# Optimization experiments

Measured on AMD Instinct MI355X. Metric: run time of the kernel, lower is better.

Reference implementation:

```python
import jax, jax.numpy as jnp
import numpy as np

D = 1024
H = 16
EPS = 1e-5


def setup_inputs() -> dict:
    key = jax.random.key(0)
    ks = jax.random.split(key, 6)
    B, T, d = 4, 2048, D
    s = 0.02
    return {
        "x": jax.random.normal(ks[0], (B, T, d), jnp.float32),
        "w_attn": jax.random.normal(ks[1], (d, 3 * d), jnp.float32) * s,
        "w_o": jax.random.normal(ks[2], (d, d), jnp.float32) * s,
        "ln1_g": jnp.ones((d,), jnp.float32),
        "ln1_b": jnp.zeros((d,), jnp.float32),
        "ln2_g": jnp.ones((d,), jnp.float32),
        "ln2_b": jnp.zeros((d,), jnp.float32),
        "w_fc": jax.random.normal(ks[3], (d, 4 * d), jnp.float32) * s,
        "b_fc": jnp.zeros((4 * d,), jnp.float32),
        "w_proj": jax.random.normal(ks[4], (4 * d, d), jnp.float32) * s,
        "b_proj": jnp.zeros((d,), jnp.float32),
    }


def _layernorm(x, g, b):
    mu = jnp.mean(x, axis=-1, keepdims=True)
    var = jnp.mean(jnp.square(x - mu), axis=-1, keepdims=True)
    return (x - mu) * jax.lax.rsqrt(var + EPS) * g + b


def _attention(x, w_attn, w_o):
    B, T, d = x.shape
    hd = d // H
    qkv = x @ w_attn  # [B,T,3d]
    q, k, v = jnp.split(qkv, 3, axis=-1)
    q = q.reshape(B, T, H, hd).transpose(0, 2, 1, 3)  # [B,H,T,hd]
    k = k.reshape(B, T, H, hd).transpose(0, 2, 1, 3)
    v = v.reshape(B, T, H, hd).transpose(0, 2, 1, 3)
    att = jnp.einsum("bhqd,bhkd->bhqk", q, k) * (1.0 / np.sqrt(hd))
    mask = jnp.tril(jnp.ones((T, T), bool))
    att = jnp.where(mask, att, jnp.float32(-jnp.inf))
    att = jax.nn.softmax(att, axis=-1)
    y = jnp.einsum("bhqk,bhkd->bhqd", att, v)
    y = y.transpose(0, 2, 1, 3).reshape(B, T, d)
    return y @ w_o


def reference(x, w_attn, w_o, ln1_g, ln1_b, ln2_g, ln2_b, w_fc, b_fc, w_proj, b_proj):
    x = x + _attention(_layernorm(x, ln1_g, ln1_b), w_attn, w_o)
    h = _layernorm(x, ln2_g, ln2_b)
    h = jax.nn.gelu(h @ w_fc + b_fc, approximate=True)
    return x + h @ w_proj + b_proj
```

## Files before the change

kernel.cpp:

```cpp
#include <hip/hip_runtime.h>
#include <math.h>

#define D_MODEL 1024
#define NHEAD   16
#define HDIM    64
#define SEQ     2048
#define BATCH   4
#define NROWS   (BATCH*SEQ)

using bf16x8 = __attribute__((ext_vector_type(8))) short;
using bf16x4 = __attribute__((ext_vector_type(4))) short;
using f32x4  = __attribute__((ext_vector_type(4))) float;

__device__ __forceinline__ unsigned short f2bf(float f) {
    unsigned u = __float_as_uint(f);
    u += 0x7fffu + ((u >> 16) & 1u);
    return (unsigned short)(u >> 16);
}
__device__ __forceinline__ float bf2f(unsigned short h) {
    unsigned u = ((unsigned)h) << 16;
    return __uint_as_float(u);
}

#define ASYNC_COPY16(g, l) \
    __builtin_amdgcn_global_load_lds((__attribute__((address_space(1))) const void*)(g), \
                                     (__attribute__((address_space(3))) void*)(l), 16, 0, 0)

__global__ __launch_bounds__(256) void ln_kernel(const float* __restrict__ x,
                                                 const float* __restrict__ g,
                                                 const float* __restrict__ b,
                                                 unsigned short* __restrict__ out) {
    const int row = blockIdx.x;
    const int tid = threadIdx.x;
    const float4* x4 = (const float4*)(x + (size_t)row * D_MODEL);
    float4 v = x4[tid];
    float s  = v.x + v.y + v.z + v.w;
    float sq = v.x*v.x + v.y*v.y + v.z*v.z + v.w*v.w;
    #pragma unroll
    for (int off = 32; off >= 1; off >>= 1) {
        s  += __shfl_down(s,  off, 64);
        sq += __shfl_down(sq, off, 64);
    }
    __shared__ float rs[4], rq[4];
    const int wave = tid >> 6;
    if ((tid & 63) == 0) { rs[wave] = s; rq[wave] = sq; }
    __syncthreads();
    const float tot  = rs[0] + rs[1] + rs[2] + rs[3];
    const float totq = rq[0] + rq[1] + rq[2] + rq[3];
    const float mu   = tot * (1.0f / D_MODEL);
    const float var  = totq * (1.0f / D_MODEL) - mu * mu;
    const float rstd = rsqrtf(var + 1e-5f);
    const float4 gv = ((const float4*)g)[tid];
    const float4 bv = ((const float4*)b)[tid];
    unsigned short* o = out + (size_t)row * D_MODEL + tid * 4;
    o[0] = f2bf((v.x - mu) * rstd * gv.x + bv.x);
    o[1] = f2bf((v.y - mu) * rstd * gv.y + bv.y);
    o[2] = f2bf((v.z - mu) * rstd * gv.z + bv.z);
    o[3] = f2bf((v.w - mu) * rstd * gv.w + bv.w);
}

__global__ __launch_bounds__(256) void wt_kernel(const float* __restrict__ w,
                                                 unsigned short* __restrict__ wt,
                                                 int K, int N) {
    __shared__ float tile[32][33];
    const int n0 = blockIdx.x * 32, k0 = blockIdx.y * 32;
    const int tx = threadIdx.x & 31, ty = threadIdx.x >> 5;
    #pragma unroll
    for (int j = 0; j < 4; ++j)
        tile[ty + j * 8][tx] = w[(size_t)(k0 + ty + j * 8) * N + n0 + tx];
    __syncthreads();
    #pragma unroll
    for (int j = 0; j < 4; ++j)
        wt[(size_t)(n0 + ty + j * 8) * K + k0 + tx] = f2bf(tile[tx][ty + j * 8]);
}

template<bool GELU, bool OUT_BF16, bool QSCALE, bool PARTIAL>
__global__ __launch_bounds__(256) void gemm_bt(const unsigned short* __restrict__ A,
                                               const unsigned short* __restrict__ Bt,
                                               const float* __restrict__ bias,
                                               const float* __restrict__ resid,
                                               void* __restrict__ outp,
                                               int M, int N, int K, int Kslice) {
    __shared__ __align__(16) unsigned short As[128 * 32];
    __shared__ __align__(16) unsigned short Bs[128 * 32];

    const int tid  = threadIdx.x;
    const int lane = tid & 63;
    const int wave = __builtin_amdgcn_readfirstlane(tid >> 6);
    const int quad = lane >> 4, l16 = lane & 15;
    const int wm = wave >> 1, wn = wave & 1;
    const int m0 = blockIdx.y * 128, n0 = blockIdx.x * 128;
    const int kbeg = PARTIAL ? blockIdx.z * Kslice : 0;

    f32x4 acc[4][4] = {};

    const int rA = tid >> 2;
    const int p  = tid & 3;
    const int cs = (p ^ ((rA >> 1) & 3)) * 8;

    const unsigned short* Ag0 = A  + (size_t)(m0 + rA) * K + cs + kbeg;
    const unsigned short* Ag1 = A  + (size_t)(m0 + rA + 64) * K + cs + kbeg;
    const unsigned short* Bg0 = Bt + (size_t)(n0 + rA) * K + cs + kbeg;
    const unsigned short* Bg1 = Bt + (size_t)(n0 + rA + 64) * K + cs + kbeg;
    unsigned short* Al0 = As + tid * 8;
    unsigned short* Al1 = As + tid * 8 + 2048;
    unsigned short* Bl0 = Bs + tid * 8;
    unsigned short* Bl1 = Bs + tid * 8 + 2048;

    const int sw = (quad ^ ((l16 >> 1) & 3)) * 8;

    for (int kb = 0; kb < Kslice; kb += 32) {
        ASYNC_COPY16(Ag0 + kb, Al0);
        ASYNC_COPY16(Ag1 + kb, Al1);
        ASYNC_COPY16(Bg0 + kb, Bl0);
        ASYNC_COPY16(Bg1 + kb, Bl1);
        __syncthreads();

        bf16x8 a[4], b[4];
        #pragma unroll
        for (int i = 0; i < 4; ++i)
            a[i] = *(const bf16x8*)&As[(wm * 64 + i * 16 + l16) * 32 + sw];
        #pragma unroll
        for (int j = 0; j < 4; ++j)
            b[j] = *(const bf16x8*)&Bs[(wn * 64 + j * 16 + l16) * 32 + sw];
        #pragma unroll
        for (int i = 0; i < 4; ++i)
            #pragma unroll
            for (int j = 0; j < 4; ++j)
                acc[i][j] = __builtin_amdgcn_mfma_f32_16x16x32_bf16(a[i], b[j], acc[i][j], 0, 0, 0);
        __syncthreads();
    }

    unsigned short* outb = (unsigned short*)outp;
    if (PARTIAL) outb += (size_t)blockIdx.z * M * N;

    #pragma unroll
    for (int i = 0; i < 4; ++i)
      #pragma unroll
      for (int j = 0; j < 4; ++j)
        #pragma unroll
        for (int r = 0; r < 4; ++r) {
            const int row = m0 + wm * 64 + i * 16 + quad * 4 + r;
            const int col = n0 + wn * 64 + j * 16 + l16;
            float v = acc[i][j][r];
            if (PARTIAL) {
                outb[(size_t)row * N + col] = f2bf(v);
            } else {
                if (QSCALE && col < 1024) v *= 0.125f;
                if (bias) v += bias[col];
                if (GELU) {
                    const float u = 0.7978845608028654f * (v + 0.044715f * v * v * v);
                    const float e = __expf(2.0f * u);
                    v = 0.5f * v * (2.0f - 2.0f / (e + 1.0f));
                }
                if (resid) v += resid[(size_t)row * N + col];
                if (OUT_BF16) outb[(size_t)row * N + col] = f2bf(v);
                else          ((float*)outp)[(size_t)row * N + col] = v;
            }
        }
}

__global__ __launch_bounds__(256, 2) void gemm_big(const unsigned short* __restrict__ A,
                                                   const unsigned short* __restrict__ Bt,
                                                   const float* __restrict__ bias,
                                                   unsigned short* __restrict__ outb,
                                                   int M, int N, int K) {
    __shared__ __align__(16) unsigned short As[256 * 32];
    __shared__ __align__(16) unsigned short Bs[128 * 32];

    const int tid  = threadIdx.x;
    const int lane = tid & 63;
    const int wave = __builtin_amdgcn_readfirstlane(tid >> 6);
    const int quad = lane >> 4, l16 = lane & 15;
    const int wm = wave >> 1, wn = wave & 1;
    const int m0 = blockIdx.y * 256, n0 = blockIdx.x * 128;

    f32x4 acc[8][4] = {};

    const int rr = tid >> 2;
    const int p  = tid & 3;
    const int cs = (p ^ ((rr >> 1) & 3)) * 8;

    const unsigned short* Ag[4];
    const unsigned short* Bg[2];
    #pragma unroll
    for (int i = 0; i < 4; ++i)
        Ag[i] = A + (size_t)(m0 + i * 64 + rr) * K + cs;
    #pragma unroll
    for (int i = 0; i < 2; ++i)
        Bg[i] = Bt + (size_t)(n0 + i * 64 + rr) * K + cs;

    const int sw = (quad ^ ((l16 >> 1) & 3)) * 8;

    for (int kb = 0; kb < K; kb += 32) {
        #pragma unroll
        for (int i = 0; i < 4; ++i)
            ASYNC_COPY16(Ag[i] + kb, As + i * 2048 + tid * 8);
        #pragma unroll
        for (int i = 0; i < 2; ++i)
            ASYNC_COPY16(Bg[i] + kb, Bs + i * 2048 + tid * 8);
        __syncthreads();

        bf16x8 b[4];
        #pragma unroll
        for (int j = 0; j < 4; ++j)
            b[j] = *(const bf16x8*)&Bs[(wn * 64 + j * 16 + l16) * 32 + sw];
        #pragma unroll
        for (int i = 0; i < 8; ++i) {
            bf16x8 a = *(const bf16x8*)&As[(wm * 128 + i * 16 + l16) * 32 + sw];
            #pragma unroll
            for (int j = 0; j < 4; ++j)
                acc[i][j] = __builtin_amdgcn_mfma_f32_16x16x32_bf16(a, b[j], acc[i][j], 0, 0, 0);
        }
        __syncthreads();
    }

    #pragma unroll
    for (int i = 0; i < 8; ++i)
      #pragma unroll
      for (int j = 0; j < 4; ++j)
        #pragma unroll
        for (int r = 0; r < 4; ++r) {
            const int row = m0 + wm * 128 + i * 16 + quad * 4 + r;
            const int col = n0 + wn * 64 + j * 16 + l16;
            float v = acc[i][j][r] + bias[col];
            const float u = 0.7978845608028654f * (v + 0.044715f * v * v * v);
            const float e = __expf(2.0f * u);
            v = 0.5f * v * (2.0f - 2.0f / (e + 1.0f));
            outb[(size_t)row * N + col] = f2bf(v);
        }
}

__global__ __launch_bounds__(256) void reduce_kernel(float* __restrict__ out,
                                                     const unsigned short* __restrict__ p0,
                                                     const unsigned short* __restrict__ p1,
                                                     const float* __restrict__ bias) {
    const int row = blockIdx.x;
    const int c0 = threadIdx.x * 4;
    const size_t base = (size_t)row * D_MODEL + c0;
    float4 o = *(float4*)(out + base);
    ushort4 a = *(const ushort4*)(p0 + base);
    ushort4 b = *(const ushort4*)(p1 + base);
    const float4 bs = *(const float4*)(bias + c0);
    o.x += bs.x + bf2f(a.x) + bf2f(b.x);
    o.y += bs.y + bf2f(a.y) + bf2f(b.y);
    o.z += bs.z + bf2f(a.z) + bf2f(b.z);
    o.w += bs.w + bf2f(a.w) + bf2f(b.w);
    *(float4*)(out + base) = o;
}

__global__ __launch_bounds__(256) void attn_kernel(const unsigned short* __restrict__ qk,
                                                   const unsigned short* __restrict__ VT,
                                                   unsigned short* __restrict__ y) {
    __shared__ __align__(16) unsigned short Qs[128 * 64];
    __shared__ __align__(16) unsigned short Ks[64 * 64];
    __shared__ __align__(16) unsigned short Vs[80 * 64];
    __shared__ __align__(16) unsigned short Ps[128 * 68];

    const int tid  = threadIdx.x;
    const int lane = tid & 63, w = tid >> 6;
    const int quad = lane >> 4, l16 = lane & 15;
    const int s7   = l16 & 7;
    const int pc0  = (quad ^ s7) * 8;
    const int pc1  = ((quad + 4) ^ s7) * 8;
    const int srow = tid >> 3, sp = tid & 7;

    const int pairidx = blockIdx.x;
    const int bh = blockIdx.y;
    const int b = bh >> 4, h = bh & 15;
    const size_t rowbase = (size_t)b * SEQ;
    const unsigned short* Qbase = qk + h * 64;
    const unsigned short* Kbase = qk + 1024 + h * 64;
    const unsigned short* Vbase = VT + (size_t)(h * 64) * NROWS + b * SEQ;

    #pragma unroll
    for (int e = 0; e < 4; ++e) {
        const int off = tid * 4 + e;
        Vs[4096 + off] = (off < 64) ? (unsigned short)0x3F80 : (unsigned short)0;
    }

    for (int phase = 0; phase < 2; ++phase) {
        const int Q = phase ? pairidx : (15 - pairidx);
        const int nkt = 2 * Q + 2;
        const int qg0 = Q * 128;

        #pragma unroll
        for (int i = 0; i < 4; ++i) {
            const int row = i * 32 + srow;
            const int c = sp ^ (row & 7);
            ASYNC_COPY16(Qbase + (rowbase + qg0 + row) * 2048 + c * 8,
                         (char*)Qs + i * 4096 + tid * 16);
        }
        __syncthreads();

        bf16x8 aq[2][2];
        #pragma unroll
        for (int sub = 0; sub < 2; ++sub) {
            const int qrow = sub * 64 + w * 16 + l16;
            aq[sub][0] = *(const bf16x8*)&Qs[qrow * 64 + pc0];
            aq[sub][1] = *(const bf16x8*)&Qs[qrow * 64 + pc1];
        }

        f32x4 o[2][5] = {};

        for (int kt = 0; kt < nkt; ++kt) {
            #pragma unroll
            for (int i = 0; i < 2; ++i) {
                const int row = i * 32 + srow;
                const int c = sp ^ (row & 7);
                ASYNC_COPY16(Kbase + (rowbase + kt * 64 + row) * 2048 + c * 8,
                             (char*)Ks + i * 4096 + tid * 16);
                ASYNC_COPY16(Vbase + (size_t)row * NROWS + kt * 64 + c * 8,
                             (char*)Vs + i * 4096 + tid * 16);
            }
            __syncthreads();

            bf16x8 bk[4][2];
            #pragma unroll
            for (int cb = 0; cb < 4; ++cb) {
                const int krow = cb * 16 + l16;
                bk[cb][0] = *(const bf16x8*)&Ks[krow * 64 + pc0];
                bk[cb][1] = *(const bf16x8*)&Ks[krow * 64 + pc1];
            }

            #pragma unroll
            for (int sub = 0; sub < 2; ++sub) {
                if (kt > 2 * Q + sub) continue;
                f32x4 s[4] = {};
                #pragma unroll
                for (int cb = 0; cb < 4; ++cb) {
                    s[cb] = __builtin_amdgcn_mfma_f32_16x16x32_bf16(aq[sub][0], bk[cb][0], s[cb], 0, 0, 0);
                    s[cb] = __builtin_amdgcn_mfma_f32_16x16x32_bf16(aq[sub][1], bk[cb][1], s[cb], 0, 0, 0);
                }
                const int prow0 = sub * 64 + w * 16 + quad * 4;
                if (kt == 2 * Q + sub) {
                    const int qg = qg0 + prow0;
                    const int kg = kt * 64 + l16;
                    #pragma unroll
                    for (int cb = 0; cb < 4; ++cb)
                        #pragma unroll
                        for (int r = 0; r < 4; ++r) {
                            const float e = __expf(s[cb][r]);
                            const float pv = (kg + cb * 16 > qg + r) ? 0.0f : e;
                            Ps[(prow0 + r) * 68 + cb * 16 + l16] = f2bf(pv);
                        }
                } else {
                    #pragma unroll
                    for (int cb = 0; cb < 4; ++cb)
                        #pragma unroll
                        for (int r = 0; r < 4; ++r)
                            Ps[(prow0 + r) * 68 + cb * 16 + l16] = f2bf(__expf(s[cb][r]));
                }
            }
            __syncthreads();

            bf16x8 bv[5][2];
            #pragma unroll
            for (int db = 0; db < 5; ++db) {
                const int vrow = db * 16 + l16;
                bv[db][0] = *(const bf16x8*)&Vs[vrow * 64 + pc0];
                bv[db][1] = *(const bf16x8*)&Vs[vrow * 64 + pc1];
            }
            #pragma unroll
            for (int sub = 0; sub < 2; ++sub) {
                if (kt > 2 * Q + sub) continue;
                const unsigned short* pb = &Ps[(sub * 64 + w * 16 + l16) * 68];
                bf16x8 ap0, ap1;
                *(bf16x4*)&ap0       = *(const bf16x4*)(pb + quad * 8);
                *((bf16x4*)&ap0 + 1) = *(const bf16x4*)(pb + quad * 8 + 4);
                *(bf16x4*)&ap1       = *(const bf16x4*)(pb + 32 + quad * 8);
                *((bf16x4*)&ap1 + 1) = *(const bf16x4*)(pb + 32 + quad * 8 + 4);
                #pragma unroll
                for (int db = 0; db < 5; ++db) {
                    o[sub][db] = __builtin_amdgcn_mfma_f32_16x16x32_bf16(ap0, bv[db][0], o[sub][db], 0, 0, 0);
                    o[sub][db] = __builtin_amdgcn_mfma_f32_16x16x32_bf16(ap1, bv[db][1], o[sub][db], 0, 0, 0);
                }
            }
            __syncthreads();
        }

        #pragma unroll
        for (int sub = 0; sub < 2; ++sub)
            #pragma unroll
            for (int r = 0; r < 4; ++r) {
                const float lsum = __shfl(o[sub][4][r], lane & 48);
                const float rinv = 1.0f / lsum;
                const int trow = qg0 + sub * 64 + w * 16 + quad * 4 + r;
                unsigned short* yp = y + (rowbase + trow) * (size_t)D_MODEL + h * 64 + l16;
                #pragma unroll
                for (int db = 0; db < 4; ++db)
                    yp[db * 16] = f2bf(o[sub][db][r] * rinv);
            }
    }
}

extern "C" void kernel_launch(void* const* d_in, const int* in_sizes, int n_in,
                              void* d_out, int out_size, void* d_ws, size_t ws_size,
                              hipStream_t stream) {
    (void)in_sizes; (void)n_in; (void)out_size; (void)ws_size;
    const float* x      = (const float*)d_in[0];
    const float* w_attn = (const float*)d_in[1];
    const float* w_o    = (const float*)d_in[2];
    const float* ln1_g  = (const float*)d_in[3];
    const float* ln1_b  = (const float*)d_in[4];
    const float* ln2_g  = (const float*)d_in[5];
    const float* ln2_b  = (const float*)d_in[6];
    const float* w_fc   = (const float*)d_in[7];
    const float* b_fc   = (const float*)d_in[8];
    const float* w_proj = (const float*)d_in[9];
    const float* b_proj = (const float*)d_in[10];
    float* out = (float*)d_out;

    char* ws = (char*)d_ws;
    unsigned short* ln_buf = (unsigned short*)ws;
    unsigned short* qkbuf  = (unsigned short*)(ws + (size_t)16  * 1048576);
    unsigned short* VTbuf  = (unsigned short*)(ws + (size_t)48  * 1048576);
    unsigned short* hbuf   = (unsigned short*)(ws + (size_t)64  * 1048576);
    unsigned short* wt_attn = hbuf;
    unsigned short* wt_o    = hbuf + (size_t)3072 * 1024;
    unsigned short* wt_fc   = qkbuf;
    unsigned short* wt_proj = qkbuf + (size_t)4096 * 1024;
    unsigned short* pbuf    = (unsigned short*)(ws + (size_t)32 * 1048576);

    wt_kernel<<<dim3(3072 / 32, 1024 / 32), 256, 0, stream>>>(w_attn, wt_attn, 1024, 3072);
    wt_kernel<<<dim3(1024 / 32, 1024 / 32), 256, 0, stream>>>(w_o, wt_o, 1024, 1024);

    ln_kernel<<<NROWS, 256, 0, stream>>>(x, ln1_g, ln1_b, ln_buf);
    gemm_bt<false, true, true, false><<<dim3(2048 / 128, NROWS / 128), 256, 0, stream>>>(
        ln_buf, wt_attn, nullptr, nullptr, qkbuf, NROWS, 2048, 1024, 1024);
    gemm_bt<false, true, false, false><<<dim3(NROWS / 128, 1024 / 128), 256, 0, stream>>>(
        wt_attn + (size_t)2048 * 1024, ln_buf, nullptr, nullptr, VTbuf, 1024, NROWS, 1024, 1024);

    attn_kernel<<<dim3(8, BATCH * NHEAD), 256, 0, stream>>>(qkbuf, VTbuf, ln_buf);

    gemm_bt<false, false, false, false><<<dim3(1024 / 128, NROWS / 128), 256, 0, stream>>>(
        ln_buf, wt_o, nullptr, x, d_out, NROWS, 1024, 1024, 1024);

    ln_kernel<<<NROWS, 256, 0, stream>>>(out, ln2_g, ln2_b, ln_buf);

    wt_kernel<<<dim3(4096 / 32, 1024 / 32), 256, 0, stream>>>(w_fc, wt_fc, 1024, 4096);
    wt_kernel<<<dim3(1024 / 32, 4096 / 32), 256, 0, stream>>>(w_proj, wt_proj, 4096, 1024);

    gemm_big<<<dim3(4096 / 128, NROWS / 256), 256, 0, stream>>>(
        ln_buf, wt_fc, b_fc, hbuf, NROWS, 4096, 1024);

    gemm_bt<false, true, false, true><<<dim3(1024 / 128, NROWS / 128, 2), 256, 0, stream>>>(
        hbuf, wt_proj, nullptr, nullptr, pbuf, NROWS, 1024, 4096, 2048);
    reduce_kernel<<<NROWS, 256, 0, stream>>>(
        out, pbuf, pbuf + (size_t)NROWS * 1024, b_proj);
}
```

Before: 587.6 us.

## Fuse QKV GEMMs into one kernel and split-K the W_o GEMM with fused LN2

Replaces the two QKV GEMM launches (QK row-major plus a separate transposed V GEMM) with one gemm_qkv kernel. It writes Q/K scaled and V transposed straight from the epilogue. The output projection GEMM now uses split-K by 4 with bf16 partials, and a new reduce kernel sums the partials with the residual and applies LayerNorm 2 in the same pass. This removes a launch and a separate LN pass and raises parallelism for the small W_o GEMM, at the cost of extra partial-buffer traffic and bf16 rounding of the partial sums.

Result: no change. 578.3 us (-1.6%).

```diff
diff --git a/kernel.cpp b/kernel.cpp
--- a/kernel.cpp
+++ b/kernel.cpp
@@ -74,7 +74,88 @@
         wt[(size_t)(n0 + ty + j * 8) * K + k0 + tx] = f2bf(tile[tx][ty + j * 8]);
 }
 
-template<bool GELU, bool OUT_BF16, bool QSCALE, bool PARTIAL>
+__global__ __launch_bounds__(256) void gemm_qkv(const unsigned short* __restrict__ A,
+                                                const unsigned short* __restrict__ Bt,
+                                                unsigned short* __restrict__ qk_out,
+                                                unsigned short* __restrict__ vt_out) {
+    const int K = 1024;
+    __shared__ __align__(16) unsigned short As[128 * 32];
+    __shared__ __align__(16) unsigned short Bs[128 * 32];
+
+    const int tid  = threadIdx.x;
+    const int lane = tid & 63;
+    const int wave = __builtin_amdgcn_readfirstlane(tid >> 6);
+    const int quad = lane >> 4, l16 = lane & 15;
+    const int wm = wave >> 1, wn = wave & 1;
+    const int m0 = blockIdx.y * 128, n0 = blockIdx.x * 128;
+
+    f32x4 acc[4][4] = {};
+
+    const int rA = tid >> 2;
+    const int p  = tid & 3;
+    const int cs = (p ^ ((rA >> 1) & 3)) * 8;
+
+    const unsigned short* Ag0 = A  + (size_t)(m0 + rA) * K + cs;
+    const unsigned short* Ag1 = A  + (size_t)(m0 + rA + 64) * K + cs;
+    const unsigned short* Bg0 = Bt + (size_t)(n0 + rA) * K + cs;
+    const unsigned short* Bg1 = Bt + (size_t)(n0 + rA + 64) * K + cs;
+    unsigned short* Al0 = As + tid * 8;
+    unsigned short* Al1 = As + tid * 8 + 2048;
+    unsigned short* Bl0 = Bs + tid * 8;
+    unsigned short* Bl1 = Bs + tid * 8 + 2048;
+
+    const int sw = (quad ^ ((l16 >> 1) & 3)) * 8;
+
+    for (int kb = 0; kb < K; kb += 32) {
+        ASYNC_COPY16(Ag0 + kb, Al0);
+        ASYNC_COPY16(Ag1 + kb, Al1);
+        ASYNC_COPY16(Bg0 + kb, Bl0);
+        ASYNC_COPY16(Bg1 + kb, Bl1);
+        __syncthreads();
+
+        bf16x8 a[4], b[4];
+        #pragma unroll
+        for (int i = 0; i < 4; ++i)
+            a[i] = *(const bf16x8*)&As[(wm * 64 + i * 16 + l16) * 32 + sw];
+        #pragma unroll
+        for (int j = 0; j < 4; ++j)
+            b[j] = *(const bf16x8*)&Bs[(wn * 64 + j * 16 + l16) * 32 + sw];
+        #pragma unroll
+        for (int i = 0; i < 4; ++i)
+            #pragma unroll
+            for (int j = 0; j < 4; ++j)
+                acc[i][j] = __builtin_amdgcn_mfma_f32_16x16x32_bf16(a[i], b[j], acc[i][j], 0, 0, 0);
+        __syncthreads();
+    }
+
+    if (n0 < 2048) {
+        const float sc = (n0 < 1024) ? 0.125f : 1.0f;
+        #pragma unroll
+        for (int i = 0; i < 4; ++i)
+          #pragma unroll
+          for (int j = 0; j < 4; ++j)
+            #pragma unroll
+            for (int r = 0; r < 4; ++r) {
+                const int row = m0 + wm * 64 + i * 16 + quad * 4 + r;
+                const int col = n0 + wn * 64 + j * 16 + l16;
+                qk_out[(size_t)row * 2048 + col] = f2bf(acc[i][j][r] * sc);
+            }
+    } else {
+        #pragma unroll
+        for (int i = 0; i < 4; ++i)
+          #pragma unroll
+          for (int j = 0; j < 4; ++j) {
+                const int dv  = n0 - 2048 + wn * 64 + j * 16 + l16;
+                const int tok = m0 + wm * 64 + i * 16 + quad * 4;
+                ushort4 pk;
+                pk.x = f2bf(acc[i][j][0]); pk.y = f2bf(acc[i][j][1]);
+                pk.z = f2bf(acc[i][j][2]); pk.w = f2bf(acc[i][j][3]);
+                *(ushort4*)(vt_out + (size_t)dv * NROWS + tok) = pk;
+            }
+    }
+}
+
+template<bool GELU, bool OUT_BF16, bool PARTIAL>
 __global__ __launch_bounds__(256) void gemm_bt(const unsigned short* __restrict__ A,
                                                const unsigned short* __restrict__ Bt,
                                                const float* __restrict__ bias,
@@ -146,7 +227,6 @@
             if (PARTIAL) {
                 outb[(size_t)row * N + col] = f2bf(v);
             } else {
-                if (QSCALE && col < 1024) v *= 0.125f;
                 if (bias) v += bias[col];
                 if (GELU) {
                     const float u = 0.7978845608028654f * (v + 0.044715f * v * v * v);
@@ -229,6 +309,49 @@
             v = 0.5f * v * (2.0f - 2.0f / (e + 1.0f));
             outb[(size_t)row * N + col] = f2bf(v);
         }
+}
+
+__global__ __launch_bounds__(256) void reduce_wo_ln2(const float* __restrict__ x,
+                                                     const unsigned short* __restrict__ pw,
+                                                     const float* __restrict__ g,
+                                                     const float* __restrict__ bb,
+                                                     float* __restrict__ out,
+                                                     unsigned short* __restrict__ lnout) {
+    const int row = blockIdx.x;
+    const int tid = threadIdx.x;
+    const size_t base = (size_t)row * D_MODEL + tid * 4;
+    const size_t stride = (size_t)NROWS * D_MODEL;
+    float4 v = *(const float4*)(x + base);
+    #pragma unroll
+    for (int z = 0; z < 4; ++z) {
+        ushort4 a = *(const ushort4*)(pw + z * stride + base);
+        v.x += bf2f(a.x); v.y += bf2f(a.y); v.z += bf2f(a.z); v.w += bf2f(a.w);
+    }
+    *(float4*)(out + base) = v;
+
+    float s  = v.x + v.y + v.z + v.w;
+    float sq = v.x*v.x + v.y*v.y + v.z*v.z + v.w*v.w;
+    #pragma unroll
+    for (int off = 32; off >= 1; off >>= 1) {
+        s  += __shfl_down(s,  off, 64);
+        sq += __shfl_down(sq, off, 64);
+    }
+    __shared__ float rs[4], rq[4];
+    const int wave = tid >> 6;
+    if ((tid & 63) == 0) { rs[wave] = s; rq[wave] = sq; }
+    __syncthreads();
+    const float tot  = rs[0] + rs[1] + rs[2] + rs[3];
+    const float totq = rq[0] + rq[1] + rq[2] + rq[3];
+    const float mu   = tot * (1.0f / D_MODEL);
+    const float var  = totq * (1.0f / D_MODEL) - mu * mu;
+    const float rstd = rsqrtf(var + 1e-5f);
+    const float4 gv = ((const float4*)g)[tid];
+    const float4 bv = ((const float4*)bb)[tid];
+    unsigned short* o = lnout + (size_t)row * D_MODEL + tid * 4;
+    o[0] = f2bf((v.x - mu) * rstd * gv.x + bv.x);
+    o[1] = f2bf((v.y - mu) * rstd * gv.y + bv.y);
+    o[2] = f2bf((v.z - mu) * rstd * gv.z + bv.z);
+    o[3] = f2bf((v.w - mu) * rstd * gv.w + bv.w);
 }
 
 __global__ __launch_bounds__(256) void reduce_kernel(float* __restrict__ out,
@@ -412,31 +535,31 @@
     float* out = (float*)d_out;
 
     char* ws = (char*)d_ws;
-    unsigned short* ln_buf = (unsigned short*)ws;
-    unsigned short* qkbuf  = (unsigned short*)(ws + (size_t)16  * 1048576);
-    unsigned short* VTbuf  = (unsigned short*)(ws + (size_t)48  * 1048576);
-    unsigned short* hbuf   = (unsigned short*)(ws + (size_t)64  * 1048576);
-    unsigned short* wt_attn = hbuf;
-    unsigned short* wt_o    = hbuf + (size_t)3072 * 1024;
-    unsigned short* wt_fc   = qkbuf;
-    unsigned short* wt_proj = qkbuf + (size_t)4096 * 1024;
-    unsigned short* pbuf    = (unsigned short*)(ws + (size_t)32 * 1048576);
+    const size_t MiB = 1048576;
+    unsigned short* ln_buf  = (unsigned short*)ws;
+    unsigned short* qkbuf   = (unsigned short*)(ws + 16 * MiB);
+    unsigned short* VTbuf   = (unsigned short*)(ws + 48 * MiB);
+    unsigned short* wt_attn = (unsigned short*)(ws + 64 * MiB);
+    unsigned short* hbuf    = (unsigned short*)(ws + 64 * MiB);
+    unsigned short* wt_o    = (unsigned short*)(ws + 126 * MiB);
+    unsigned short* pw      = (unsigned short*)(ws + 16 * MiB);
+    unsigned short* wt_fc   = (unsigned short*)(ws + 16 * MiB);
+    unsigned short* wt_proj = (unsigned short*)(ws + 24 * MiB);
+    unsigned short* pp      = (unsigned short*)(ws + 32 * MiB);
 
     wt_kernel<<<dim3(3072 / 32, 1024 / 32), 256, 0, stream>>>(w_attn, wt_attn, 1024, 3072);
     wt_kernel<<<dim3(1024 / 32, 1024 / 32), 256, 0, stream>>>(w_o, wt_o, 1024, 1024);
 
     ln_kernel<<<NROWS, 256, 0, stream>>>(x, ln1_g, ln1_b, ln_buf);
-    gemm_bt<false, true, true, false><<<dim3(2048 / 128, NROWS / 128), 256, 0, stream>>>(
-        ln_buf, wt_attn, nullptr, nullptr, qkbuf, NROWS, 2048, 1024, 1024);
-    gemm_bt<false, true, false, false><<<dim3(NROWS / 128, 1024 / 128), 256, 0, stream>>>(
-        wt_attn + (size_t)2048 * 1024, ln_buf, nullptr, nullptr, VTbuf, 1024, NROWS, 1024, 1024);
+
+    gemm_qkv<<<dim3(3072 / 128, NROWS / 128), 256, 0, stream>>>(
+        ln_buf, wt_attn, qkbuf, VTbuf);
 
     attn_kernel<<<dim3(8, BATCH * NHEAD), 256, 0, stream>>>(qkbuf, VTbuf, ln_buf);
 
-    gemm_bt<false, false, false, false><<<dim3(1024 / 128, NROWS / 128), 256, 0, stream>>>(
-        ln_buf, wt_o, nullptr, x, d_out, NROWS, 1024, 1024, 1024);
-
-    ln_kernel<<<NROWS, 256, 0, stream>>>(out, ln2_g, ln2_b, ln_buf);
+    gemm_bt<false, true, true><<<dim3(1024 / 128, NROWS / 128, 4), 256, 0, stream>>>(
+        ln_buf, wt_o, nullptr, nullptr, pw, NROWS, 1024, 1024, 256);
+    reduce_wo_ln2<<<NROWS, 256, 0, stream>>>(x, pw, ln2_g, ln2_b, out, ln_buf);
 
     wt_kernel<<<dim3(4096 / 32, 1024 / 32), 256, 0, stream>>>(w_fc, wt_fc, 1024, 4096);
     wt_kernel<<<dim3(1024 / 32, 4096 / 32), 256, 0, stream>>>(w_proj, wt_proj, 4096, 1024);
@@ -444,8 +567,8 @@
     gemm_big<<<dim3(4096 / 128, NROWS / 256), 256, 0, stream>>>(
         ln_buf, wt_fc, b_fc, hbuf, NROWS, 4096, 1024);
 
-    gemm_bt<false, true, false, true><<<dim3(1024 / 128, NROWS / 128, 2), 256, 0, stream>>>(
-        hbuf, wt_proj, nullptr, nullptr, pbuf, NROWS, 1024, 4096, 2048);
+    gemm_bt<false, true, true><<<dim3(1024 / 128, NROWS / 128, 2), 256, 0, stream>>>(
+        hbuf, wt_proj, nullptr, nullptr, pp, NROWS, 1024, 4096, 2048);
     reduce_kernel<<<NROWS, 256, 0, stream>>>(
-        out, pbuf, pbuf + (size_t)NROWS * 1024, b_proj);
-}
+        out, pp, pp + (size_t)NROWS * 1024, b_proj);
+}
```
